# Performance work log

Measured on AMD Instinct MI355X. Metric: run time of the kernel, lower is better.

The kernel has to match this reference:

```python
import jax, jax.numpy as jnp
import numpy as np

IN_F = 4096
OUT_F = 4096
NNZ = 1_600_000
BATCH = 512


def setup_inputs() -> dict:
    key = jax.random.key(0)
    k_x, k_w, k_b, k_r, k_c = jax.random.split(key, 5)
    x = jax.random.normal(k_x, (BATCH, IN_F), dtype=jnp.float32)
    weight1d = jax.random.normal(k_w, (NNZ,), dtype=jnp.float32) * 0.02
    bias = jax.random.normal(k_b, (OUT_F,), dtype=jnp.float32) * 0.02
    row_idx = jax.random.randint(k_r, (NNZ,), 0, OUT_F, dtype=jnp.int64 if jax.config.jax_enable_x64 else jnp.int32)
    col_idx = jax.random.randint(k_c, (NNZ,), 0, IN_F, dtype=jnp.int64 if jax.config.jax_enable_x64 else jnp.int32)
    return {
        "x": x,
        "weight1d": weight1d,
        "bias": bias,
        "row_idx": row_idx,
        "col_idx": col_idx,
        "in_f": IN_F,
        "out_f": OUT_F,
    }


def reference(x, weight1d, bias, row_idx, col_idx, in_f, out_f):
    # matching torch advanced-index assignment semantics up to duplicate ordering).
    W = jnp.zeros((out_f, in_f), dtype=weight1d.dtype).at[row_idx, col_idx].set(weight1d)
    # F.linear(x, W, bias) = x @ W.T + bias
    return x @ W.T + bias
```

## Files before the change

kernel.cpp:

```cpp
#include <hip/hip_runtime.h>
#include <hip/hip_bf16.h>

typedef unsigned short u16;
typedef unsigned long long u64;
typedef __attribute__((ext_vector_type(4))) float f32x4;
typedef __attribute__((ext_vector_type(8))) short bf16x8;

#define IN_F   4096
#define OUT_F  4096
#define BATCH  512

#define BM 128
#define BN 128
#define BK 64
#define KSPLIT 4
#define KC (IN_F / KSPLIT)
#define NSTEPS (KC / BK)

#define NXCD    8
#define NB      256
#define CHUNK   2048
#define LCAP    24
#define SEGCAP  2048
#define RCAP    640
#define GOVFCAP (1024*1024)
#define OVF2CAP (128*1024)
#define NCTR    (NXCD * NB + 2)

__device__ inline u16 f2bf(float f) {
    __hip_bfloat16 h = __float2bfloat16(f);
    u16 u; __builtin_memcpy(&u, &h, 2); return u;
}

__global__ __launch_bounds__(256) void conv_x(const float* __restrict__ x,
                                              u16* __restrict__ xbf,
                                              int* __restrict__ ctrs) {
    const int tid = threadIdx.x;
    if (blockIdx.x == 0) {
        for (int j = tid; j < NCTR; j += 256) ctrs[j] = 0;
    }
    int i = blockIdx.x * 256 + tid;
    float4 v = ((const float4*)x)[i];
    ushort4 o;
    o.x = f2bf(v.x); o.y = f2bf(v.y); o.z = f2bf(v.z); o.w = f2bf(v.w);
    ((ushort4*)xbf)[i] = o;
}

__global__ __launch_bounds__(256) void bucket_scatter(const int* __restrict__ row,
                                                      const int* __restrict__ col,
                                                      const float* __restrict__ w,
                                                      int* __restrict__ gcur,
                                                      u64* __restrict__ bins,
                                                      int* __restrict__ govf_cnt,
                                                      u64* __restrict__ govf, int nnz) {
    __shared__ u64 lbin[NB][LCAP];
    __shared__ int lcur[NB];
    const int xcd = __builtin_amdgcn_s_getreg(20 | (3 << 11)) & (NXCD - 1);
    const int tid = threadIdx.x;
    lcur[tid] = 0;
    __syncthreads();

    int base = blockIdx.x * CHUNK + tid * 8;
    if (base + 8 <= nnz) {
        int4 r0 = ((const int4*)(row + base))[0];
        int4 r1 = ((const int4*)(row + base))[1];
        int4 c0 = ((const int4*)(col + base))[0];
        int4 c1 = ((const int4*)(col + base))[1];
        float4 w0 = ((const float4*)(w + base))[0];
        float4 w1 = ((const float4*)(w + base))[1];
        int rs[8] = {r0.x, r0.y, r0.z, r0.w, r1.x, r1.y, r1.z, r1.w};
        int cs[8] = {c0.x, c0.y, c0.z, c0.w, c1.x, c1.y, c1.z, c1.w};
        float wsv[8] = {w0.x, w0.y, w0.z, w0.w, w1.x, w1.y, w1.z, w1.w};
#pragma unroll
        for (int j = 0; j < 8; j++) {
            int rr = rs[j], cc = cs[j], i = base + j;
            u64 wb = (u64)f2bf(wsv[j]);
            int bk = rr >> 4;
            int p = atomicAdd(&lcur[bk], 1);
            if (p < LCAP) {
                lbin[bk][p] = ((u64)i << 32) | ((u64)(rr & 15) << 28) | ((u64)cc << 16) | wb;
            } else {
                int o = atomicAdd(govf_cnt, 1);
                if (o < GOVFCAP) govf[o] = ((u64)i << 40) | ((u64)rr << 28) | ((u64)cc << 16) | wb;
            }
        }
    } else {
        int e = nnz < base + 8 ? nnz : base + 8;
        for (int i = base; i < e; i++) {
            int rr = row[i], cc = col[i];
            u64 wb = (u64)f2bf(w[i]);
            int bk = rr >> 4;
            int p = atomicAdd(&lcur[bk], 1);
            if (p < LCAP) {
                lbin[bk][p] = ((u64)i << 32) | ((u64)(rr & 15) << 28) | ((u64)cc << 16) | wb;
            } else {
                int o = atomicAdd(govf_cnt, 1);
                if (o < GOVFCAP) govf[o] = ((u64)i << 40) | ((u64)rr << 28) | ((u64)cc << 16) | wb;
            }
        }
    }
    __syncthreads();

    int cnt = lcur[tid];
    if (cnt > LCAP) cnt = LCAP;
    if (cnt > 0) {
        int gb = (xcd << 8) | tid;
        int b0 = atomicAdd(&gcur[gb], cnt);
        u64* seg = bins + (size_t)gb * SEGCAP;
        for (int k = 0; k < cnt; k++) {
            u64 e = lbin[tid][k];
            int p = b0 + k;
            if (p < SEGCAP) {
                seg[p] = e;
            } else {
                int rr = (tid << 4) | ((int)(e >> 28) & 15);
                int o = atomicAdd(govf_cnt, 1);
                if (o < GOVFCAP) govf[o] = ((e >> 32) << 40) | ((u64)rr << 28) | (e & 0x0FFFFFFF);
            }
        }
    }
}

__global__ __launch_bounds__(256) void split_bucket(const int* __restrict__ gcur,
                                                    const u64* __restrict__ bins,
                                                    const int* __restrict__ govf_cnt,
                                                    const u64* __restrict__ govf,
                                                    u64* __restrict__ rowbins,
                                                    int* __restrict__ rowcnt,
                                                    int* __restrict__ ovf2_cnt,
                                                    u64* __restrict__ ovf2) {
    __shared__ u64 lists[16][RCAP];
    __shared__ int lcur[16];
    const int bucket = blockIdx.x;
    const int tid = threadIdx.x;
    if (tid < 16) lcur[tid] = 0;
    __syncthreads();

#pragma unroll
    for (int xcd = 0; xcd < NXCD; xcd++) {
        int gb = (xcd << 8) | bucket;
        int cnt = gcur[gb];
        if (cnt > SEGCAP) cnt = SEGCAP;
        const u64* seg = bins + (size_t)gb * SEGCAP;
        for (int k = tid; k < cnt; k += 256) {
            u64 e = seg[k];
            int rl = (int)(e >> 28) & 15;
            int p = atomicAdd(&lcur[rl], 1);
            if (p < RCAP) lists[rl][p] = e;
            else {
                int rr = (bucket << 4) | rl;
                int o = atomicAdd(ovf2_cnt, 1);
                if (o < OVF2CAP) ovf2[o] = ((e >> 32) << 40) | ((u64)rr << 28) | (e & 0x0FFFFFFF);
            }
        }
    }
    int ovfn = *govf_cnt;
    if (ovfn > GOVFCAP) ovfn = GOVFCAP;
    for (int k = tid; k < ovfn; k += 256) {
        u64 e = govf[k];
        int rr = (int)(e >> 28) & 4095;
        if ((rr >> 4) == bucket) {
            u64 e2 = ((e >> 40) << 32) | ((u64)(rr & 15) << 28) | (e & 0x0FFFFFFF);
            int rl = rr & 15;
            int p = atomicAdd(&lcur[rl], 1);
            if (p < RCAP) lists[rl][p] = e2;
            else { int o = atomicAdd(ovf2_cnt, 1); if (o < OVF2CAP) ovf2[o] = ((e2 >> 32) << 40) | ((u64)rr << 28) | (e2 & 0x0FFFFFFF); }
        }
    }
    __syncthreads();

    for (int rl = 0; rl < 16; rl++) {
        int cnt = lcur[rl];
        if (cnt > RCAP) cnt = RCAP;
        int rowg = (bucket << 4) | rl;
        u64* dst = rowbins + (size_t)rowg * RCAP;
        for (int k = tid; k < cnt; k += 256) dst[k] = lists[rl][k];
        if (tid == 0) rowcnt[rowg] = cnt;
    }
}

__global__ __launch_bounds__(256) void build_row2(const u64* __restrict__ rowbins,
                                                  const int* __restrict__ rowcnt,
                                                  const int* __restrict__ ovf2_cnt,
                                                  const u64* __restrict__ ovf2,
                                                  u16* __restrict__ Wbf) {
    __shared__ u64 aux[IN_F];
    const int rowg = blockIdx.x;
    const int tid = threadIdx.x;

#pragma unroll
    for (int j = 0; j < IN_F / 256 / 2; j++)
        ((ulonglong2*)aux)[tid * 8 + j] = (ulonglong2){0ull, 0ull};
    __syncthreads();

    int cnt = rowcnt[rowg];
    const u64* seg = rowbins + (size_t)rowg * RCAP;
    for (int k = tid; k < cnt; k += 256) {
        u64 e = seg[k];
        atomicMax(&aux[(int)(e >> 16) & 4095], ((e >> 32) << 16) | (e & 0xFFFF));
    }
    int o2 = *ovf2_cnt;
    if (o2 > OVF2CAP) o2 = OVF2CAP;
    for (int k = tid; k < o2; k += 256) {
        u64 e = ovf2[k];
        if (((int)(e >> 28) & 4095) == rowg)
            atomicMax(&aux[(int)(e >> 16) & 4095], ((e >> 40) << 16) | (e & 0xFFFF));
    }
    __syncthreads();

    int base = tid * 16;
    ushort4 o[4];
#pragma unroll
    for (int j = 0; j < 16; j++)
        ((u16*)o)[j] = (u16)(aux[base + j] & 0xFFFF);
    uint4* dst = (uint4*)(Wbf + (size_t)rowg * IN_F + base);
    dst[0] = ((const uint4*)o)[0];
    dst[1] = ((const uint4*)o)[1];
}

__global__ __launch_bounds__(256) void gemm_part(const u16* __restrict__ A,
                                                 const u16* __restrict__ B,
                                                 float* __restrict__ part) {
    __shared__ u16 As[2][BM * BK];
    __shared__ u16 Bs[2][BN * BK];
    const int L   = blockIdx.x;
    const int xx  = L & 7;
    const int rst = L >> 3;
    const int m   = rst & 3;
    const int g   = ((rst >> 2) << 3) | xx;
    const int n   = g & 31;
    const int kc  = g >> 5;
    const int m0  = m * BM;
    const int n0  = n * BN;
    const int kt0 = kc * KC;

    const int tid  = threadIdx.x;
    const int lane = tid & 63;
    const int wave = tid >> 6;
    const int wm = wave >> 1, wn = wave & 1;
    const int r15 = lane & 15, khi = lane >> 4;

    const u16* srcA[4]; const u16* srcB[4]; int dstO[4];
#pragma unroll
    for (int it = 0; it < 4; it++) {
        int o = tid * 16 + it * 4096;
        int rr = o >> 7, lblk = (o >> 4) & 7;
        srcA[it] = A + (size_t)(m0 + rr) * IN_F + kt0 + ((lblk ^ (rr & 7)) << 3);
        srcB[it] = B + (size_t)(n0 + rr) * IN_F + kt0 + ((lblk ^ (rr & 7)) << 3);
        dstO[it] = o >> 1;
    }

#define STAGE(buf, kk)                                                               \
    do {                                                                             \
        _Pragma("unroll")                                                            \
        for (int it = 0; it < 4; it++)                                               \
            __builtin_amdgcn_global_load_lds(                                        \
                (const __attribute__((address_space(1))) void*)(srcA[it] + (kk)),    \
                (__attribute__((address_space(3))) void*)(&As[buf][dstO[it]]),       \
                16, 0, 0);                                                           \
        _Pragma("unroll")                                                            \
        for (int it = 0; it < 4; it++)                                               \
            __builtin_amdgcn_global_load_lds(                                        \
                (const __attribute__((address_space(1))) void*)(srcB[it] + (kk)),    \
                (__attribute__((address_space(3))) void*)(&Bs[buf][dstO[it]]),       \
                16, 0, 0);                                                           \
    } while (0)

    f32x4 acc[4][4];
#pragma unroll
    for (int mi = 0; mi < 4; mi++)
#pragma unroll
        for (int nj = 0; nj < 4; nj++) acc[mi][nj] = (f32x4){0.f, 0.f, 0.f, 0.f};

    STAGE(0, 0);

    for (int t = 0; t < NSTEPS; ++t) {
        const int cur = t & 1;
        if (t + 1 < NSTEPS) {
            STAGE(cur ^ 1, (t + 1) * BK);
            asm volatile("s_waitcnt vmcnt(8)" ::: "memory");
        } else {
            asm volatile("s_waitcnt vmcnt(0)" ::: "memory");
        }
        __builtin_amdgcn_s_barrier();

        const char* as = (const char*)&As[cur][0];
        const char* bs = (const char*)&Bs[cur][0];
#pragma unroll
        for (int ks = 0; ks < 2; ks++) {
            bf16x8 a[4], b[4];
#pragma unroll
            for (int mi = 0; mi < 4; mi++) {
                int rowi = wm * 64 + mi * 16 + r15;
                a[mi] = *(const bf16x8*)(as + rowi * 128 + (((ks * 4 + khi) ^ (rowi & 7)) << 4));
            }
#pragma unroll
            for (int nj = 0; nj < 4; nj++) {
                int rowi = wn * 64 + nj * 16 + r15;
                b[nj] = *(const bf16x8*)(bs + rowi * 128 + (((ks * 4 + khi) ^ (rowi & 7)) << 4));
            }
#pragma unroll
            for (int mi = 0; mi < 4; mi++)
#pragma unroll
                for (int nj = 0; nj < 4; nj++)
                    acc[mi][nj] = __builtin_amdgcn_mfma_f32_16x16x32_bf16(a[mi], b[nj], acc[mi][nj], 0, 0, 0);
        }
        __builtin_amdgcn_s_barrier();
    }
#undef STAGE

    float* P = part + (size_t)kc * BATCH * OUT_F;
#pragma unroll
    for (int nj = 0; nj < 4; nj++) {
        int colg = n0 + wn * 64 + nj * 16 + r15;
#pragma unroll
        for (int mi = 0; mi < 4; mi++) {
#pragma unroll
            for (int j = 0; j < 4; j++) {
                int rowg = m0 + wm * 64 + mi * 16 + khi * 4 + j;
                P[(size_t)rowg * OUT_F + colg] = acc[mi][nj][j];
            }
        }
    }
}

__global__ __launch_bounds__(256) void reduce_bias(const float* __restrict__ part,
                                                   const float* __restrict__ bias,
                                                   float* __restrict__ y) {
    int i = blockIdx.x * 256 + threadIdx.x;
    const size_t STRIDE = (size_t)BATCH * OUT_F / 4;
    f32x4 s = ((const f32x4*)part)[i];
#pragma unroll
    for (int k = 1; k < KSPLIT; k++) s += ((const f32x4*)part)[i + k * STRIDE];
    int col4 = (i * 4) & (OUT_F - 1);
    f32x4 b = *(const f32x4*)&bias[col4];
    ((f32x4*)y)[i] = s + b;
}

extern "C" void kernel_launch(void* const* d_in, const int* in_sizes, int n_in,
                              void* d_out, int out_size, void* d_ws, size_t ws_size,
                              hipStream_t stream) {
    const float* x    = (const float*)d_in[0];
    const float* w1d  = (const float*)d_in[1];
    const float* bias = (const float*)d_in[2];
    const int*   row  = (const int*)d_in[3];
    const int*   col  = (const int*)d_in[4];
    const int nnz = in_sizes[1];

    char* ws        = (char*)d_ws;
    u64*  bins      = (u64*)ws;
    float* part     = (float*)ws;
    int*  gcur      = (int*)(ws + ((size_t)32 << 20));
    int*  govf_cnt  = gcur + NXCD * NB;
    int*  ovf2_cnt  = govf_cnt + 1;
    u64*  govf      = (u64*)(ws + ((size_t)33 << 20));
    u64*  rowbins   = (u64*)(ws + ((size_t)41 << 20));
    int*  rowcnt    = (int*)(ws + ((size_t)61 << 20));
    u64*  ovf2      = (u64*)(ws + ((size_t)62 << 20));
    u16*  Wbf       = (u16*)(ws + ((size_t)64 << 20));
    u16*  xbf       = (u16*)(ws + ((size_t)96 << 20));
    float* y        = (float*)d_out;

    conv_x<<<(BATCH * IN_F / 4) / 256, 256, 0, stream>>>(x, xbf, gcur);
    int nblk = (nnz + CHUNK - 1) / CHUNK;
    bucket_scatter<<<nblk, 256, 0, stream>>>(row, col, w1d, gcur, bins, govf_cnt, govf, nnz);
    split_bucket<<<NB, 256, 0, stream>>>(gcur, bins, govf_cnt, govf, rowbins, rowcnt, ovf2_cnt, ovf2);
    build_row2<<<OUT_F, 256, 0, stream>>>(rowbins, rowcnt, ovf2_cnt, ovf2, Wbf);
    gemm_part<<<512, 256, 0, stream>>>(xbf, Wbf, part);
    reduce_bias<<<(BATCH * OUT_F / 4) / 256, 256, 0, stream>>>(part, bias, y);
}
```

Before: 102.9 us.

## Fuse split-K reduction and bias into GEMM with last-block tile counters

The GEMM tile grows to 256x128 with 512 threads, so 256 blocks cover the problem in a single wave. The separate reduce_bias kernel is removed. Instead, each output tile keeps an atomic counter, and the last of the four split-K blocks to finish sums the partial results and adds the bias. This saves a kernel launch and gives better operand reuse per block. In exchange, only 64 blocks do the reduction at the tail, fences are added, the XCD-aware block swizzle is dropped, and per-block LDS use is larger.

```diff
diff --git a/kernel.cpp b/kernel.cpp
--- a/kernel.cpp
+++ b/kernel.cpp
@@ -10,12 +10,13 @@
 #define OUT_F  4096
 #define BATCH  512
 
-#define BM 128
+#define BM 256
 #define BN 128
 #define BK 64
 #define KSPLIT 4
 #define KC (IN_F / KSPLIT)
 #define NSTEPS (KC / BK)
+#define NTILES ((BATCH / BM) * (OUT_F / BN))
 
 #define NXCD    8
 #define NB      256
@@ -25,7 +26,7 @@
 #define RCAP    640
 #define GOVFCAP (1024*1024)
 #define OVF2CAP (128*1024)
-#define NCTR    (NXCD * NB + 2)
+#define NCTR    (NXCD * NB + 2 + NTILES)
 
 __device__ inline u16 f2bf(float f) {
     __hip_bfloat16 h = __float2bfloat16(f);
@@ -218,18 +219,19 @@
     dst[1] = ((const uint4*)o)[1];
 }
 
-__global__ __launch_bounds__(256) void gemm_part(const u16* __restrict__ A,
-                                                 const u16* __restrict__ B,
-                                                 float* __restrict__ part) {
+__global__ __launch_bounds__(512) void gemm_fused(const u16* __restrict__ A,
+                                                  const u16* __restrict__ B,
+                                                  const float* __restrict__ bias,
+                                                  float* __restrict__ part,
+                                                  int* __restrict__ tilectr,
+                                                  float* __restrict__ y) {
     __shared__ u16 As[2][BM * BK];
     __shared__ u16 Bs[2][BN * BK];
+    __shared__ int done_s;
     const int L   = blockIdx.x;
-    const int xx  = L & 7;
-    const int rst = L >> 3;
-    const int m   = rst & 3;
-    const int g   = ((rst >> 2) << 3) | xx;
-    const int n   = g & 31;
-    const int kc  = g >> 5;
+    const int n   = L >> 3;
+    const int m   = (L & 7) >> 2;
+    const int kc  = L & 3;
     const int m0  = m * BM;
     const int n0  = n * BN;
     const int kt0 = kc * KC;
@@ -240,14 +242,21 @@
     const int wm = wave >> 1, wn = wave & 1;
     const int r15 = lane & 15, khi = lane >> 4;
 
-    const u16* srcA[4]; const u16* srcB[4]; int dstO[4];
+    const u16* srcA[4]; int dstA[4];
+    const u16* srcB[2]; int dstB[2];
 #pragma unroll
     for (int it = 0; it < 4; it++) {
-        int o = tid * 16 + it * 4096;
+        int o = tid * 16 + it * 8192;
         int rr = o >> 7, lblk = (o >> 4) & 7;
         srcA[it] = A + (size_t)(m0 + rr) * IN_F + kt0 + ((lblk ^ (rr & 7)) << 3);
+        dstA[it] = o >> 1;
+    }
+#pragma unroll
+    for (int it = 0; it < 2; it++) {
+        int o = tid * 16 + it * 8192;
+        int rr = o >> 7, lblk = (o >> 4) & 7;
         srcB[it] = B + (size_t)(n0 + rr) * IN_F + kt0 + ((lblk ^ (rr & 7)) << 3);
-        dstO[it] = o >> 1;
+        dstB[it] = o >> 1;
     }
 
 #define STAGE(buf, kk)                                                               \
@@ -256,13 +265,13 @@
         for (int it = 0; it < 4; it++)                                               \
             __builtin_amdgcn_global_load_lds(                                        \
                 (const __attribute__((address_space(1))) void*)(srcA[it] + (kk)),    \
-                (__attribute__((address_space(3))) void*)(&As[buf][dstO[it]]),       \
+                (__attribute__((address_space(3))) void*)(&As[buf][dstA[it]]),       \
                 16, 0, 0);                                                           \
         _Pragma("unroll")                                                            \
-        for (int it = 0; it < 4; it++)                                               \
+        for (int it = 0; it < 2; it++)                                               \
             __builtin_amdgcn_global_load_lds(                                        \
                 (const __attribute__((address_space(1))) void*)(srcB[it] + (kk)),    \
-                (__attribute__((address_space(3))) void*)(&Bs[buf][dstO[it]]),       \
+                (__attribute__((address_space(3))) void*)(&Bs[buf][dstB[it]]),       \
                 16, 0, 0);                                                           \
     } while (0)
 
@@ -278,7 +287,7 @@
         const int cur = t & 1;
         if (t + 1 < NSTEPS) {
             STAGE(cur ^ 1, (t + 1) * BK);
-            asm volatile("s_waitcnt vmcnt(8)" ::: "memory");
+            asm volatile("s_waitcnt vmcnt(6)" ::: "memory");
         } else {
             asm volatile("s_waitcnt vmcnt(0)" ::: "memory");
         }
@@ -322,19 +331,30 @@
             }
         }
     }
-}
-
-__global__ __launch_bounds__(256) void reduce_bias(const float* __restrict__ part,
-                                                   const float* __restrict__ bias,
-                                                   float* __restrict__ y) {
-    int i = blockIdx.x * 256 + threadIdx.x;
-    const size_t STRIDE = (size_t)BATCH * OUT_F / 4;
-    f32x4 s = ((const f32x4*)part)[i];
-#pragma unroll
-    for (int k = 1; k < KSPLIT; k++) s += ((const f32x4*)part)[i + k * STRIDE];
-    int col4 = (i * 4) & (OUT_F - 1);
-    f32x4 b = *(const f32x4*)&bias[col4];
-    ((f32x4*)y)[i] = s + b;
+
+    __threadfence();
+    __syncthreads();
+    if (tid == 0) {
+        int old = atomicAdd(&tilectr[m * (OUT_F / BN) + n], 1);
+        done_s = (old == KSPLIT - 1) ? 1 : 0;
+    }
+    __syncthreads();
+    if (done_s) {
+        __threadfence();
+        const size_t S = (size_t)BATCH * OUT_F / 4;
+#pragma unroll 4
+        for (int j = 0; j < (BM * BN / 4) / 512; j++) {
+            int li = j * 512 + tid;
+            int r  = li >> 5;
+            int c4 = li & 31;
+            size_t base4 = ((size_t)(m0 + r) * OUT_F + n0) / 4 + c4;
+            f32x4 s = ((const f32x4*)part)[base4];
+#pragma unroll
+            for (int k = 1; k < KSPLIT; k++) s += ((const f32x4*)part)[base4 + k * S];
+            f32x4 b = *(const f32x4*)&bias[n0 + c4 * 4];
+            ((f32x4*)y)[base4] = s + b;
+        }
+    }
 }
 
 extern "C" void kernel_launch(void* const* d_in, const int* in_sizes, int n_in,
@@ -353,6 +373,7 @@
     int*  gcur      = (int*)(ws + ((size_t)32 << 20));
     int*  govf_cnt  = gcur + NXCD * NB;
     int*  ovf2_cnt  = govf_cnt + 1;
+    int*  tilectr   = ovf2_cnt + 1;
     u64*  govf      = (u64*)(ws + ((size_t)33 << 20));
     u64*  rowbins   = (u64*)(ws + ((size_t)41 << 20));
     int*  rowcnt    = (int*)(ws + ((size_t)61 << 20));
@@ -366,6 +387,5 @@
     bucket_scatter<<<nblk, 256, 0, stream>>>(row, col, w1d, gcur, bins, govf_cnt, govf, nnz);
     split_bucket<<<NB, 256, 0, stream>>>(gcur, bins, govf_cnt, govf, rowbins, rowcnt, ovf2_cnt, ovf2);
     build_row2<<<OUT_F, 256, 0, stream>>>(rowbins, rowcnt, ovf2_cnt, ovf2, Wbf);
-    gemm_part<<<512, 256, 0, stream>>>(xbf, Wbf, part);
-    reduce_bias<<<(BATCH * OUT_F / 4) / 256, 256, 0, stream>>>(part, bias, y);
-}
+    gemm_fused<<<(BATCH / BM) * (OUT_F / BN) * KSPLIT, 512, 0, stream>>>(xbf, Wbf, bias, part, tilectr, y);
+}
```

Result: slower. 196.3 us (+90.7%).
